# Kernel tuning notes

Measured on AMD Instinct MI355X. Metric: run time of the kernel, lower is better.

Reference implementation:

```python
import jax, jax.numpy as jnp
import numpy as np

TEMPERATURE = 8.0  # sqrt(k_dim=64)
NEG = -2.0 ** 15   # masked_fill value from the torch module


def setup_inputs() -> dict:
    key = jax.random.key(0)
    kq, kk, kv, km = jax.random.split(key, 4)
    B, H, N, L, D = 4, 8, 128, 128, 64
    q = jax.random.normal(kq, (B, H, N, L, D), dtype=jnp.float32)
    k = jax.random.normal(kk, (B, H, N, L, D), dtype=jnp.float32)
    v = jax.random.normal(kv, (B, H, N, L, D), dtype=jnp.float32)
    mask = jax.random.randint(km, (B, 1, N, L, L), 0, 2, dtype=jnp.int32)
    return {"q": q, "k": k, "v": v, "mask": mask}


def reference(q, k, v, mask):
    # attn: [B,H,N,Lq,Lk] = q [B,H,N,Lq,D] @ k^T [B,H,N,D,Lk]
    attn = jnp.einsum('bhnqd,bhnkd->bhnqk', q, k) / TEMPERATURE
    attn = jnp.where(mask == 0, jnp.float32(NEG), attn)
    attn = jax.nn.softmax(attn, axis=-1)
    # dropout is identity in eval mode
    out = jnp.einsum('bhnqk,bhnkd->bhnqd', attn, v)
    return out
```

## Files before the change

### kernel.cpp

```cpp
#include <hip/hip_runtime.h>
#include <hip/hip_bf16.h>


typedef __bf16 bf16;
typedef bf16 bf16x4 __attribute__((ext_vector_type(4)));
typedef bf16 bf16x8 __attribute__((ext_vector_type(8)));
typedef float f32x4 __attribute__((ext_vector_type(4)));

#define MFMA16(a, b, c) __builtin_amdgcn_mfma_f32_16x16x32_bf16((a), (b), (c), 0, 0, 0)

__global__ __launch_bounds__(256, 4) void attn_head_kernel(
    const float* __restrict__ q, const float* __restrict__ k,
    const float* __restrict__ v, const int* __restrict__ mask,
    float* __restrict__ out)
{
    constexpr int H = 8, N = 128, L = 128, D = 64;

    __shared__ __align__(16) char SMEM[35840];
    bf16 (*KL)[72]  = (bf16(*)[72])SMEM;
    bf16 (*VT)[136] = (bf16(*)[136])(SMEM + 18432);

    int bid  = blockIdx.x;
    int lidx = (bid & 7) * 512 + (bid >> 3);
    int h = lidx & 7, n = (lidx >> 3) & 127, b = lidx >> 10;

    const size_t base = (((size_t)(b * H + h)) * N + n) * (size_t)(L * D);
    const float* Qp = q + base;
    const float* Kp = k + base;
    const float* Vp = v + base;
    float*       Op = out + base;
    const int*   Mp = mask + ((size_t)(b * N + n)) * (size_t)(L * L);

    const int tid  = threadIdx.x;
    const int wave = tid >> 6;
    const int lane = tid & 63;
    const int g    = lane >> 4;
    const int c    = lane & 15;

    #pragma unroll
    for (int i = 0; i < 8; ++i) {
        int e   = i * 256 + tid;
        int row = e >> 4;
        int d0  = (e & 15) * 4;
        float4 kv = ((const float4*)Kp)[e];
        bf16x4 pk = { (bf16)kv.x, (bf16)kv.y, (bf16)kv.z, (bf16)kv.w };
        *(bf16x4*)&KL[row][d0] = pk;
    }
    #pragma unroll
    for (int i = 0; i < 2; ++i) {
        int id = i * 256 + tid;
        int db = id & 15;
        int kb = id >> 4;
        const float4* vp = (const float4*)(Vp + kb * 4 * 64 + db * 4);
        float4 r0 = vp[0], r1 = vp[16], r2 = vp[32], r3 = vp[48];
        bf16x4 w0 = { (bf16)r0.x, (bf16)r1.x, (bf16)r2.x, (bf16)r3.x };
        bf16x4 w1 = { (bf16)r0.y, (bf16)r1.y, (bf16)r2.y, (bf16)r3.y };
        bf16x4 w2 = { (bf16)r0.z, (bf16)r1.z, (bf16)r2.z, (bf16)r3.z };
        bf16x4 w3 = { (bf16)r0.w, (bf16)r1.w, (bf16)r2.w, (bf16)r3.w };
        *(bf16x4*)&VT[db * 4 + 0][kb * 4] = w0;
        *(bf16x4*)&VT[db * 4 + 1][kb * 4] = w1;
        *(bf16x4*)&VT[db * 4 + 2][kb * 4] = w2;
        *(bf16x4*)&VT[db * 4 + 3][kb * 4] = w3;
    }

    bf16x8 qb[2][2];
    #pragma unroll
    for (int rt = 0; rt < 2; ++rt)
        #pragma unroll
        for (int ds = 0; ds < 2; ++ds) {
            int row = wave * 32 + rt * 16 + c;
            const float4* p = (const float4*)(Qp + row * D + ds * 32 + g * 8);
            float4 x0 = p[0], x1 = p[1];
            bf16x8 f = { (bf16)(x0.x * 0.125f), (bf16)(x0.y * 0.125f),
                         (bf16)(x0.z * 0.125f), (bf16)(x0.w * 0.125f),
                         (bf16)(x1.x * 0.125f), (bf16)(x1.y * 0.125f),
                         (bf16)(x1.z * 0.125f), (bf16)(x1.w * 0.125f) };
            qb[rt][ds] = f;
        }

    __syncthreads();

    f32x4 acc[8][2];
    #pragma unroll
    for (int kt = 0; kt < 8; ++kt)
        #pragma unroll
        for (int rt = 0; rt < 2; ++rt)
            acc[kt][rt] = (f32x4){0.f, 0.f, 0.f, 0.f};

    #pragma unroll
    for (int kt = 0; kt < 8; ++kt) {
        bf16x8 ka0 = *(const bf16x8*)&KL[kt * 16 + c][g * 8];
        bf16x8 ka1 = *(const bf16x8*)&KL[kt * 16 + c][32 + g * 8];
        #pragma unroll
        for (int rt = 0; rt < 2; ++rt) {
            acc[kt][rt] = MFMA16(ka0, qb[rt][0], acc[kt][rt]);
            acc[kt][rt] = MFMA16(ka1, qb[rt][1], acc[kt][rt]);
        }
    }

    __syncthreads();

    float rinv[2];
    #pragma unroll
    for (int rt = 0; rt < 2; ++rt) {
        int qrow = wave * 32 + rt * 16 + c;
        const int* mrow = Mp + (size_t)qrow * L;
        int4 mm[8];
        #pragma unroll
        for (int kt = 0; kt < 8; ++kt)
            mm[kt] = *(const int4*)(mrow + kt * 16 + g * 4);
        float mx = -3.0e38f;
        #pragma unroll
        for (int kt = 0; kt < 8; ++kt) {
            float s0 = mm[kt].x ? acc[kt][rt][0] : -32768.f;
            float s1 = mm[kt].y ? acc[kt][rt][1] : -32768.f;
            float s2 = mm[kt].z ? acc[kt][rt][2] : -32768.f;
            float s3 = mm[kt].w ? acc[kt][rt][3] : -32768.f;
            acc[kt][rt][0] = s0; acc[kt][rt][1] = s1;
            acc[kt][rt][2] = s2; acc[kt][rt][3] = s3;
            mx = fmaxf(mx, fmaxf(fmaxf(s0, s1), fmaxf(s2, s3)));
        }
        mx = fmaxf(mx, __shfl_xor(mx, 16));
        mx = fmaxf(mx, __shfl_xor(mx, 32));
        float sum = 0.f;
        #pragma unroll
        for (int kt = 0; kt < 8; ++kt) {
            #pragma unroll
            for (int j = 0; j < 4; ++j) {
                float e = __expf(acc[kt][rt][j] - mx);
                acc[kt][rt][j] = e;
                sum += e;
            }
        }
        sum += __shfl_xor(sum, 16);
        sum += __shfl_xor(sum, 32);
        rinv[rt] = __builtin_amdgcn_rcpf(sum);
    }

    bf16* PLw = (bf16*)(SMEM + wave * 4608);
    f32x4 oacc[2][4];
    #pragma unroll
    for (int rt = 0; rt < 2; ++rt)
        #pragma unroll
        for (int dt = 0; dt < 4; ++dt)
            oacc[rt][dt] = (f32x4){0.f, 0.f, 0.f, 0.f};

    #pragma unroll
    for (int p = 0; p < 2; ++p) {
        #pragma unroll
        for (int rt = 0; rt < 2; ++rt) {
            float r = rinv[rt];
            #pragma unroll
            for (int t = 0; t < 4; ++t) {
                f32x4 a = acc[p * 4 + t][rt];
                bf16x4 w = { (bf16)(a[0] * r), (bf16)(a[1] * r),
                             (bf16)(a[2] * r), (bf16)(a[3] * r) };
                *(bf16x4*)&PLw[(rt * 16 + c) * 72 + t * 16 + g * 4] = w;
            }
        }
        asm volatile("s_waitcnt lgkmcnt(0)" ::: "memory");
        __builtin_amdgcn_sched_barrier(0);

        #pragma unroll
        for (int kc2 = 0; kc2 < 2; ++kc2) {
            int kc = p * 2 + kc2;
            bf16x8 vb[4];
            #pragma unroll
            for (int dt = 0; dt < 4; ++dt)
                vb[dt] = *(const bf16x8*)&VT[dt * 16 + c][kc * 32 + g * 8];
            #pragma unroll
            for (int rt = 0; rt < 2; ++rt) {
                bf16x8 pa = *(const bf16x8*)&PLw[(rt * 16 + c) * 72 + kc2 * 32 + g * 8];
                #pragma unroll
                for (int dt = 0; dt < 4; ++dt)
                    oacc[rt][dt] = MFMA16(pa, vb[dt], oacc[rt][dt]);
            }
        }
        asm volatile("" ::: "memory");
    }

    #pragma unroll
    for (int rt = 0; rt < 2; ++rt)
        #pragma unroll
        for (int j = 0; j < 4; ++j) {
            int row = wave * 32 + rt * 16 + g * 4 + j;
            float* orow = Op + row * D;
            #pragma unroll
            for (int dt = 0; dt < 4; ++dt)
                orow[dt * 16 + c] = oacc[rt][dt][j];
        }
}

extern "C" void kernel_launch(void* const* d_in, const int* in_sizes, int n_in,
                              void* d_out, int out_size, void* d_ws, size_t ws_size,
                              hipStream_t stream) {
    const float* q    = (const float*)d_in[0];
    const float* k    = (const float*)d_in[1];
    const float* v    = (const float*)d_in[2];
    const int*   mask = (const int*)d_in[3];
    float*       out  = (float*)d_out;
    attn_head_kernel<<<4096, 256, 0, stream>>>(q, k, v, mask, out);
}
```

Baseline: 118.2 us.

## Swizzle LDS layouts, use exp2 softmax, vectorize output stores, raise occupancy

Replaces the padded LDS layouts for K, V-transpose and P with XOR-swizzled unpadded layouts, which shrinks shared memory to 32KB and lets launch bounds ask for five blocks per CU. The softmax folds log2(e) into the Q scale, uses exp2, and applies the mask after exponentiation by zeroing entries. The PV MFMA operands are swapped so each lane holds four contiguous output columns, allowing float4 global stores instead of scalar ones. This risks subtle differences for fully-masked rows, where the reference gives a uniform softmax but zeroed exponents sum to zero.

```diff
diff --git a/kernel.cpp b/kernel.cpp
--- a/kernel.cpp
+++ b/kernel.cpp
@@ -3,22 +3,25 @@
 
 
 typedef __bf16 bf16;
+typedef bf16 bf16x2 __attribute__((ext_vector_type(2)));
 typedef bf16 bf16x4 __attribute__((ext_vector_type(4)));
 typedef bf16 bf16x8 __attribute__((ext_vector_type(8)));
 typedef float f32x4 __attribute__((ext_vector_type(4)));
+typedef unsigned u32;
 
 #define MFMA16(a, b, c) __builtin_amdgcn_mfma_f32_16x16x32_bf16((a), (b), (c), 0, 0, 0)
 
-__global__ __launch_bounds__(256, 4) void attn_head_kernel(
+__global__ __launch_bounds__(256, 5) void attn_head_kernel(
     const float* __restrict__ q, const float* __restrict__ k,
     const float* __restrict__ v, const int* __restrict__ mask,
     float* __restrict__ out)
 {
     constexpr int H = 8, N = 128, L = 128, D = 64;
-
-    __shared__ __align__(16) char SMEM[35840];
-    bf16 (*KL)[72]  = (bf16(*)[72])SMEM;
-    bf16 (*VT)[136] = (bf16(*)[136])(SMEM + 18432);
+    constexpr float QSCALE = 0.125f * 1.4426950408889634f;
+
+    __shared__ __align__(16) char SMEM[32768];
+    char* KB = SMEM;
+    char* VB = SMEM + 16384;
 
     int bid  = blockIdx.x;
     int lidx = (bid & 7) * 512 + (bid >> 3);
@@ -43,8 +46,9 @@
         int row = e >> 4;
         int d0  = (e & 15) * 4;
         float4 kv = ((const float4*)Kp)[e];
-        bf16x4 pk = { (bf16)kv.x, (bf16)kv.y, (bf16)kv.z, (bf16)kv.w };
-        *(bf16x4*)&KL[row][d0] = pk;
+        bf16x4 pk4 = { (bf16)kv.x, (bf16)kv.y, (bf16)kv.z, (bf16)kv.w };
+        int off = row * 128 + ((((d0 >> 3) ^ (row & 7)) << 4) | ((d0 & 4) << 1));
+        *(bf16x4*)(KB + off) = pk4;
     }
     #pragma unroll
     for (int i = 0; i < 2; ++i) {
@@ -53,14 +57,18 @@
         int kb = id >> 4;
         const float4* vp = (const float4*)(Vp + kb * 4 * 64 + db * 4);
         float4 r0 = vp[0], r1 = vp[16], r2 = vp[32], r3 = vp[48];
-        bf16x4 w0 = { (bf16)r0.x, (bf16)r1.x, (bf16)r2.x, (bf16)r3.x };
-        bf16x4 w1 = { (bf16)r0.y, (bf16)r1.y, (bf16)r2.y, (bf16)r3.y };
-        bf16x4 w2 = { (bf16)r0.z, (bf16)r1.z, (bf16)r2.z, (bf16)r3.z };
-        bf16x4 w3 = { (bf16)r0.w, (bf16)r1.w, (bf16)r2.w, (bf16)r3.w };
-        *(bf16x4*)&VT[db * 4 + 0][kb * 4] = w0;
-        *(bf16x4*)&VT[db * 4 + 1][kb * 4] = w1;
-        *(bf16x4*)&VT[db * 4 + 2][kb * 4] = w2;
-        *(bf16x4*)&VT[db * 4 + 3][kb * 4] = w3;
+        bf16x4 w[4] = {
+            { (bf16)r0.x, (bf16)r1.x, (bf16)r2.x, (bf16)r3.x },
+            { (bf16)r0.y, (bf16)r1.y, (bf16)r2.y, (bf16)r3.y },
+            { (bf16)r0.z, (bf16)r1.z, (bf16)r2.z, (bf16)r3.z },
+            { (bf16)r0.w, (bf16)r1.w, (bf16)r2.w, (bf16)r3.w } };
+        #pragma unroll
+        for (int j = 0; j < 4; ++j) {
+            int row = db * 4 + j;
+            int gr  = (kb >> 1) ^ (row & 15) ^ (row >> 2);
+            int off = row * 256 + (gr << 4) + ((kb & 1) * 8);
+            *(bf16x4*)(VB + off) = w[j];
+        }
     }
 
     bf16x8 qb[2][2];
@@ -69,13 +77,13 @@
         #pragma unroll
         for (int ds = 0; ds < 2; ++ds) {
             int row = wave * 32 + rt * 16 + c;
-            const float4* p = (const float4*)(Qp + row * D + ds * 32 + g * 8);
-            float4 x0 = p[0], x1 = p[1];
-            bf16x8 f = { (bf16)(x0.x * 0.125f), (bf16)(x0.y * 0.125f),
-                         (bf16)(x0.z * 0.125f), (bf16)(x0.w * 0.125f),
-                         (bf16)(x1.x * 0.125f), (bf16)(x1.y * 0.125f),
-                         (bf16)(x1.z * 0.125f), (bf16)(x1.w * 0.125f) };
-            qb[rt][ds] = f;
+            const float4* qp = (const float4*)(Qp + row * D + ds * 32 + g * 8);
+            float4 x0 = qp[0], x1 = qp[1];
+            qb[rt][ds] = (bf16x8){
+                (bf16)(x0.x * QSCALE), (bf16)(x0.y * QSCALE),
+                (bf16)(x0.z * QSCALE), (bf16)(x0.w * QSCALE),
+                (bf16)(x1.x * QSCALE), (bf16)(x1.y * QSCALE),
+                (bf16)(x1.z * QSCALE), (bf16)(x1.w * QSCALE) };
         }
 
     __syncthreads();
@@ -89,8 +97,9 @@
 
     #pragma unroll
     for (int kt = 0; kt < 8; ++kt) {
-        bf16x8 ka0 = *(const bf16x8*)&KL[kt * 16 + c][g * 8];
-        bf16x8 ka1 = *(const bf16x8*)&KL[kt * 16 + c][32 + g * 8];
+        int row = kt * 16 + c;
+        bf16x8 ka0 = *(const bf16x8*)(KB + row * 128 + (((g    ) ^ (row & 7)) << 4));
+        bf16x8 ka1 = *(const bf16x8*)(KB + row * 128 + (((4 + g) ^ (row & 7)) << 4));
         #pragma unroll
         for (int rt = 0; rt < 2; ++rt) {
             acc[kt][rt] = MFMA16(ka0, qb[rt][0], acc[kt][rt]);
@@ -112,32 +121,32 @@
         float mx = -3.0e38f;
         #pragma unroll
         for (int kt = 0; kt < 8; ++kt) {
-            float s0 = mm[kt].x ? acc[kt][rt][0] : -32768.f;
-            float s1 = mm[kt].y ? acc[kt][rt][1] : -32768.f;
-            float s2 = mm[kt].z ? acc[kt][rt][2] : -32768.f;
-            float s3 = mm[kt].w ? acc[kt][rt][3] : -32768.f;
-            acc[kt][rt][0] = s0; acc[kt][rt][1] = s1;
-            acc[kt][rt][2] = s2; acc[kt][rt][3] = s3;
-            mx = fmaxf(mx, fmaxf(fmaxf(s0, s1), fmaxf(s2, s3)));
+            f32x4 a = acc[kt][rt];
+            mx = fmaxf(mx, fmaxf(fmaxf(a[0], a[1]), fmaxf(a[2], a[3])));
         }
         mx = fmaxf(mx, __shfl_xor(mx, 16));
         mx = fmaxf(mx, __shfl_xor(mx, 32));
         float sum = 0.f;
         #pragma unroll
         for (int kt = 0; kt < 8; ++kt) {
-            #pragma unroll
-            for (int j = 0; j < 4; ++j) {
-                float e = __expf(acc[kt][rt][j] - mx);
-                acc[kt][rt][j] = e;
-                sum += e;
-            }
+            float e0 = __builtin_amdgcn_exp2f(acc[kt][rt][0] - mx);
+            float e1 = __builtin_amdgcn_exp2f(acc[kt][rt][1] - mx);
+            float e2 = __builtin_amdgcn_exp2f(acc[kt][rt][2] - mx);
+            float e3 = __builtin_amdgcn_exp2f(acc[kt][rt][3] - mx);
+            e0 = mm[kt].x ? e0 : 0.f;
+            e1 = mm[kt].y ? e1 : 0.f;
+            e2 = mm[kt].z ? e2 : 0.f;
+            e3 = mm[kt].w ? e3 : 0.f;
+            acc[kt][rt][0] = e0; acc[kt][rt][1] = e1;
+            acc[kt][rt][2] = e2; acc[kt][rt][3] = e3;
+            sum += (e0 + e1) + (e2 + e3);
         }
         sum += __shfl_xor(sum, 16);
         sum += __shfl_xor(sum, 32);
         rinv[rt] = __builtin_amdgcn_rcpf(sum);
     }
 
-    bf16* PLw = (bf16*)(SMEM + wave * 4608);
+    char* PW = SMEM + wave * 4096;
     f32x4 oacc[2][4];
     #pragma unroll
     for (int rt = 0; rt < 2; ++rt)
@@ -146,16 +155,19 @@
             oacc[rt][dt] = (f32x4){0.f, 0.f, 0.f, 0.f};
 
     #pragma unroll
-    for (int p = 0; p < 2; ++p) {
+    for (int pp = 0; pp < 2; ++pp) {
         #pragma unroll
         for (int rt = 0; rt < 2; ++rt) {
             float r = rinv[rt];
+            int row = rt * 16 + c;
             #pragma unroll
             for (int t = 0; t < 4; ++t) {
-                f32x4 a = acc[p * 4 + t][rt];
+                f32x4 a = acc[pp * 4 + t][rt];
                 bf16x4 w = { (bf16)(a[0] * r), (bf16)(a[1] * r),
                              (bf16)(a[2] * r), (bf16)(a[3] * r) };
-                *(bf16x4*)&PLw[(rt * 16 + c) * 72 + t * 16 + g * 4] = w;
+                int kl  = t * 16 + g * 4;
+                int off = row * 128 + ((((kl >> 3) ^ (row & 7)) << 4) | ((kl & 4) << 1));
+                *(bf16x4*)(PW + off) = w;
             }
         }
         asm volatile("s_waitcnt lgkmcnt(0)" ::: "memory");
@@ -163,32 +175,37 @@
 
         #pragma unroll
         for (int kc2 = 0; kc2 < 2; ++kc2) {
-            int kc = p * 2 + kc2;
-            bf16x8 vb[4];
+            int kc = pp * 2 + kc2;
+            bf16x8 va[4];
             #pragma unroll
-            for (int dt = 0; dt < 4; ++dt)
-                vb[dt] = *(const bf16x8*)&VT[dt * 16 + c][kc * 32 + g * 8];
+            for (int dt = 0; dt < 4; ++dt) {
+                int row = dt * 16 + c;
+                int gr  = (kc * 4 + g) ^ (row & 15) ^ (row >> 2);
+                va[dt] = *(const bf16x8*)(VB + row * 256 + (gr << 4));
+            }
             #pragma unroll
             for (int rt = 0; rt < 2; ++rt) {
-                bf16x8 pa = *(const bf16x8*)&PLw[(rt * 16 + c) * 72 + kc2 * 32 + g * 8];
+                int row = rt * 16 + c;
+                int gr  = (kc2 * 4 + g) ^ (row & 7);
+                bf16x8 pa = *(const bf16x8*)(PW + row * 128 + (gr << 4));
                 #pragma unroll
                 for (int dt = 0; dt < 4; ++dt)
-                    oacc[rt][dt] = MFMA16(pa, vb[dt], oacc[rt][dt]);
+                    oacc[rt][dt] = MFMA16(va[dt], pa, oacc[rt][dt]);
             }
         }
         asm volatile("" ::: "memory");
     }
 
     #pragma unroll
-    for (int rt = 0; rt < 2; ++rt)
-        #pragma unroll
-        for (int j = 0; j < 4; ++j) {
-            int row = wave * 32 + rt * 16 + g * 4 + j;
-            float* orow = Op + row * D;
-            #pragma unroll
-            for (int dt = 0; dt < 4; ++dt)
-                orow[dt * 16 + c] = oacc[rt][dt][j];
-        }
+    for (int rt = 0; rt < 2; ++rt) {
+        int qrow = wave * 32 + rt * 16 + c;
+        #pragma unroll
+        for (int dt = 0; dt < 4; ++dt) {
+            f32x4 o = oacc[rt][dt];
+            float4 st = { o[0], o[1], o[2], o[3] };
+            *(float4*)(Op + (size_t)qrow * D + dt * 16 + g * 4) = st;
+        }
+    }
 }
 
 extern "C" void kernel_launch(void* const* d_in, const int* in_sizes, int n_in,
```

Result: slower. 157.0 us (+32.8%).
